# Kernel optimization log

Measured on AMD Instinct MI355X. Metric: run time of the kernel, lower is better.

Reference implementation:

```python
import jax, jax.numpy as jnp
import numpy as np

EMBED_DIM = 1024
NUM_HEADS = 16
HEAD_DIM = EMBED_DIM // NUM_HEADS
WINDOW_SIZE = 256
BATCH = 2
SEQ = 2048


def setup_inputs() -> dict:
    key = jax.random.key(0)
    ks = jax.random.split(key, 5)
    s = 1.0 / np.sqrt(EMBED_DIM)
    return {
        "x": jax.random.normal(ks[0], (BATCH, SEQ, EMBED_DIM), dtype=jnp.float32),
        "Wq": jax.random.normal(ks[1], (EMBED_DIM, EMBED_DIM), dtype=jnp.float32) * s,
        "Wk": jax.random.normal(ks[2], (EMBED_DIM, EMBED_DIM), dtype=jnp.float32) * s,
        "Wv": jax.random.normal(ks[3], (EMBED_DIM, EMBED_DIM), dtype=jnp.float32) * s,
        "Wo": jax.random.normal(ks[4], (EMBED_DIM, EMBED_DIM), dtype=jnp.float32) * s,
    }


def _split_heads(t):
    # [B, S, E] -> [B, H, S, D]
    b, s, _ = t.shape
    return t.reshape(b, s, NUM_HEADS, HEAD_DIM).transpose(0, 2, 1, 3)


def reference(x, Wq, Wk, Wv, Wo):
    b, s, _ = x.shape
    # nn.Linear(bias=False): y = x @ W.T
    q = _split_heads(x @ Wq.T)
    k = _split_heads(x @ Wk.T)
    v = _split_heads(x @ Wv.T)
    scores = jnp.einsum("bhqd,bhkd->bhqk", q, k) / np.sqrt(HEAD_DIM).astype(np.float32)
    i = jnp.arange(s)[:, None]
    j = jnp.arange(s)[None, :]
    # causal sliding window: attend to j in [i - window_size + 1, i]
    allowed = (j <= i) & (j >= i - WINDOW_SIZE + 1)
    scores = jnp.where(allowed[None, None], scores, -jnp.inf)
    probs = jax.nn.softmax(scores, axis=-1)
    ctx = jnp.einsum("bhqk,bhkd->bhqd", probs, v)  # [B,H,S,D]
    ctx = ctx.transpose(0, 2, 1, 3).reshape(b, s, EMBED_DIM)
    return ctx @ Wo.T
```

## Files before the change

kernel.cpp:

```cpp
#include <hip/hip_runtime.h>
#include <hip/hip_bf16.h>
#include <stdint.h>

#define EDIM 1024
#define NH 16
#define HD 64
#define WIN 256
#define BB 2
#define SS 2048
#define MR (BB*SS)
#define NQKV 3072

typedef __attribute__((ext_vector_type(8))) short short8;
typedef __attribute__((ext_vector_type(4))) float f32x4;

__device__ __forceinline__ unsigned short f2bf(float f) {
  union { float f; uint32_t u; } c; c.f = f;
  uint32_t r = (c.u + 0x7FFFu + ((c.u >> 16) & 1u)) >> 16;
  return (unsigned short)r;
}

__global__ __launch_bounds__(256) void cvt_kernel(const float* __restrict__ s,
                                                  unsigned short* __restrict__ d, int n8) {
  int i = blockIdx.x * 256 + threadIdx.x;
  if (i >= n8) return;
  const float4* s4 = (const float4*)s;
  float4 a = s4[2*i], b = s4[2*i+1];
  short8 o;
  o[0]=(short)f2bf(a.x); o[1]=(short)f2bf(a.y); o[2]=(short)f2bf(a.z); o[3]=(short)f2bf(a.w);
  o[4]=(short)f2bf(b.x); o[5]=(short)f2bf(b.y); o[6]=(short)f2bf(b.z); o[7]=(short)f2bf(b.w);
  ((short8*)d)[i] = o;
}

template<typename OutT>
__global__ __launch_bounds__(256) void gemm_bt(const unsigned short* __restrict__ A,
                                               const unsigned short* __restrict__ Bw,
                                               OutT* __restrict__ C, int M, int N, int K) {
  __shared__ unsigned short As[128*64];
  __shared__ unsigned short Bs[128*64];
  const int t = threadIdx.x, lane = t & 63;
  const int w = t >> 6, wr = w >> 1, wc = w & 1;
  const int m0 = blockIdx.y * 128, n0 = blockIdx.x * 128;
  f32x4 acc[4][4] = {};
  for (int kt = 0; kt < K; kt += 64) {
    __syncthreads();
#pragma unroll
    for (int r = 0; r < 4; ++r) {
      const int row = r*32 + (t >> 3);
      const int colb = (((t & 7) ^ (row & 7)) << 4);
      const int o = r*4096 + t*16;
      __builtin_amdgcn_global_load_lds(
        (const __attribute__((address_space(1))) char*)(A + (size_t)(m0 + row) * K + kt + (colb >> 1)),
        (__attribute__((address_space(3))) char*)((char*)As + o), 16, 0, 0);
      __builtin_amdgcn_global_load_lds(
        (const __attribute__((address_space(1))) char*)(Bw + (size_t)(n0 + row) * K + kt + (colb >> 1)),
        (__attribute__((address_space(3))) char*)((char*)Bs + o), 16, 0, 0);
    }
    __syncthreads();
#pragma unroll
    for (int c = 0; c < 2; ++c) {
      const int k0 = c*32 + ((lane >> 4) << 3);
      short8 af[4], bfr[4];
#pragma unroll
      for (int mi = 0; mi < 4; ++mi) {
        const int row = wr*64 + mi*16 + (lane & 15);
        const int off = ((row << 7) + (k0 << 1)) ^ ((row & 7) << 4);
        af[mi] = *(const short8*)((const char*)As + off);
      }
#pragma unroll
      for (int ni = 0; ni < 4; ++ni) {
        const int row = wc*64 + ni*16 + (lane & 15);
        const int off = ((row << 7) + (k0 << 1)) ^ ((row & 7) << 4);
        bfr[ni] = *(const short8*)((const char*)Bs + off);
      }
#pragma unroll
      for (int mi = 0; mi < 4; ++mi)
#pragma unroll
        for (int ni = 0; ni < 4; ++ni)
          acc[mi][ni] = __builtin_amdgcn_mfma_f32_16x16x32_bf16(af[mi], bfr[ni], acc[mi][ni], 0, 0, 0);
    }
  }
#pragma unroll
  for (int mi = 0; mi < 4; ++mi) {
    const int rb = m0 + wr*64 + mi*16 + ((lane >> 4) << 2);
#pragma unroll
    for (int ni = 0; ni < 4; ++ni) {
      const int col = n0 + wc*64 + ni*16 + (lane & 15);
#pragma unroll
      for (int reg = 0; reg < 4; ++reg) {
        const float v = acc[mi][ni][reg];
        const size_t idx = (size_t)(rb + reg) * N + col;
        if constexpr (sizeof(OutT) == 2) ((unsigned short*)C)[idx] = f2bf(v);
        else ((float*)C)[idx] = v;
      }
    }
  }
}

__global__ __launch_bounds__(256) void attn_kernel(const unsigned short* __restrict__ qkv,
                                                   unsigned short* __restrict__ ctx) {
  __shared__ unsigned short Ks[64*64];
  __shared__ unsigned short VTs[64*64];
  __shared__ unsigned short Ps[4][16*64];
  const int t = threadIdx.x, lane = t & 63, w = t >> 6;
  const int qt = blockIdx.x, bh = blockIdx.y;
  const int b = bh >> 4, h = bh & 15;
  const int q0 = qt << 6;
  const int qw0 = q0 + (w << 4);
  const unsigned short* qb = qkv + (size_t)b * SS * NQKV + h * HD;
  const unsigned short* kb = qb + EDIM;
  const unsigned short* vb = qb + 2*EDIM;
  short8 aq[2];
  {
    const size_t roff = (size_t)(qw0 + (lane & 15)) * NQKV + ((lane >> 4) << 3);
    aq[0] = *(const short8*)(qb + roff);
    aq[1] = *(const short8*)(qb + roff + 32);
  }
  f32x4 oacc[4] = {};
  float mrun[4], lrun[4];
#pragma unroll
  for (int r = 0; r < 4; ++r) { mrun[r] = -1e30f; lrun[r] = 0.f; }
  const int t_lo = qt >= 4 ? qt - 4 : 0;
  for (int kt = t_lo; kt <= qt; ++kt) {
    const int kv0 = kt << 6;
    __syncthreads();
#pragma unroll
    for (int r = 0; r < 2; ++r) {
      const int o = r*4096 + t*16;
      const int key = o >> 7;
      const int colb = (o & 127) ^ ((key & 7) << 4);
      __builtin_amdgcn_global_load_lds(
        (const __attribute__((address_space(1))) char*)(kb + (size_t)(kv0 + key) * NQKV + (colb >> 1)),
        (__attribute__((address_space(3))) char*)((char*)Ks + o), 16, 0, 0);
    }
#pragma unroll
    for (int i = 0; i < 2; ++i) {
      const int c = t + (i << 8);
      const int key = c >> 3;
      const int d0 = (c & 7) << 3;
      short8 vv = *(const short8*)(vb + (size_t)(kv0 + key) * NQKV + d0);
#pragma unroll
      for (int j = 0; j < 8; ++j) {
        const int d = d0 + j;
        const int off = ((d << 7) + (key << 1)) ^ ((d & 7) << 4);
        *(unsigned short*)((char*)VTs + off) = (unsigned short)(short)vv[j];
      }
    }
    __syncthreads();
    f32x4 sc[4] = {};
#pragma unroll
    for (int kf = 0; kf < 4; ++kf) {
#pragma unroll
      for (int c = 0; c < 2; ++c) {
        const int krow = (kf << 4) + (lane & 15);
        const int k0 = (c << 5) + ((lane >> 4) << 3);
        const int off = ((krow << 7) + (k0 << 1)) ^ ((krow & 7) << 4);
        short8 bk = *(const short8*)((const char*)Ks + off);
        sc[kf] = __builtin_amdgcn_mfma_f32_16x16x32_bf16(aq[c], bk, sc[kf], 0, 0, 0);
      }
    }
#pragma unroll
    for (int reg = 0; reg < 4; ++reg) {
      const int qg = qw0 + ((lane >> 4) << 2) + reg;
      float sv[4];
#pragma unroll
      for (int kf = 0; kf < 4; ++kf) {
        const int kg = kv0 + (kf << 4) + (lane & 15);
        const bool ok = (kg <= qg) && (kg + WIN > qg);
        sv[kf] = ok ? sc[kf][reg] * 0.125f : -1e30f;
      }
      float pm = fmaxf(fmaxf(sv[0], sv[1]), fmaxf(sv[2], sv[3]));
      pm = fmaxf(pm, __shfl_xor(pm, 1));
      pm = fmaxf(pm, __shfl_xor(pm, 2));
      pm = fmaxf(pm, __shfl_xor(pm, 4));
      pm = fmaxf(pm, __shfl_xor(pm, 8));
      const float mn = fmaxf(mrun[reg], pm);
      const float corr = __expf(mrun[reg] - mn);
      mrun[reg] = mn;
      float rs = 0.f;
      const int qrow = ((lane >> 4) << 2) + reg;
#pragma unroll
      for (int kf = 0; kf < 4; ++kf) {
        const float p = __expf(sv[kf] - mn);
        rs += p;
        const int key = (kf << 4) + (lane & 15);
        const int off = ((qrow << 7) + (key << 1)) ^ ((qrow & 7) << 4);
        *(unsigned short*)((char*)&Ps[w][0] + off) = f2bf(p);
      }
      rs += __shfl_xor(rs, 1);
      rs += __shfl_xor(rs, 2);
      rs += __shfl_xor(rs, 4);
      rs += __shfl_xor(rs, 8);
      lrun[reg] = lrun[reg] * corr + rs;
#pragma unroll
      for (int nf = 0; nf < 4; ++nf) oacc[nf][reg] *= corr;
    }
#pragma unroll
    for (int c2 = 0; c2 < 2; ++c2) {
      const int prow = lane & 15;
      const int k0 = (c2 << 5) + ((lane >> 4) << 3);
      const int offp = ((prow << 7) + (k0 << 1)) ^ ((prow & 7) << 4);
      short8 pa = *(const short8*)((const char*)&Ps[w][0] + offp);
#pragma unroll
      for (int nf = 0; nf < 4; ++nf) {
        const int d = (nf << 4) + (lane & 15);
        const int offv = ((d << 7) + (k0 << 1)) ^ ((d & 7) << 4);
        short8 bv = *(const short8*)((const char*)VTs + offv);
        oacc[nf] = __builtin_amdgcn_mfma_f32_16x16x32_bf16(pa, bv, oacc[nf], 0, 0, 0);
      }
    }
  }
  unsigned short* cb = ctx + (size_t)b * SS * EDIM + h * HD;
#pragma unroll
  for (int nf = 0; nf < 4; ++nf)
#pragma unroll
    for (int reg = 0; reg < 4; ++reg) {
      const int qg = qw0 + ((lane >> 4) << 2) + reg;
      const int d = (nf << 4) + (lane & 15);
      cb[(size_t)qg * EDIM + d] = f2bf(oacc[nf][reg] / lrun[reg]);
    }
}

extern "C" void kernel_launch(void* const* d_in, const int* in_sizes, int n_in,
                              void* d_out, int out_size, void* d_ws, size_t ws_size,
                              hipStream_t stream) {
  const float* x  = (const float*)d_in[0];
  const float* Wq = (const float*)d_in[1];
  const float* Wk = (const float*)d_in[2];
  const float* Wv = (const float*)d_in[3];
  const float* Wo = (const float*)d_in[4];
  float* out = (float*)d_out;
  char* ws = (char*)d_ws;
  unsigned short* xb   = (unsigned short*)(ws);
  unsigned short* ctxb = (unsigned short*)(ws);
  unsigned short* wqkv = (unsigned short*)(ws + (size_t)(8u << 20));
  unsigned short* wob  = (unsigned short*)(ws + (size_t)(14u << 20));
  unsigned short* qkv  = (unsigned short*)(ws + (size_t)(16u << 20));

  const int nx8 = (MR * EDIM) / 8;
  const int nw8 = (EDIM * EDIM) / 8;
  cvt_kernel<<<dim3(nx8 / 256), dim3(256), 0, stream>>>(x, xb, nx8);
  cvt_kernel<<<dim3(nw8 / 256), dim3(256), 0, stream>>>(Wq, wqkv, nw8);
  cvt_kernel<<<dim3(nw8 / 256), dim3(256), 0, stream>>>(Wk, wqkv + EDIM*EDIM, nw8);
  cvt_kernel<<<dim3(nw8 / 256), dim3(256), 0, stream>>>(Wv, wqkv + 2*EDIM*EDIM, nw8);
  cvt_kernel<<<dim3(nw8 / 256), dim3(256), 0, stream>>>(Wo, wob, nw8);

  gemm_bt<unsigned short><<<dim3(NQKV/128, MR/128), dim3(256), 0, stream>>>(
      xb, wqkv, qkv, MR, NQKV, EDIM);

  attn_kernel<<<dim3(SS/64, BB*NH), dim3(256), 0, stream>>>(qkv, ctxb);

  gemm_bt<float><<<dim3(EDIM/128, MR/128), dim3(256), 0, stream>>>(
      ctxb, wob, out, MR, EDIM, EDIM);
}
```

Baseline: 175.5 us.

## Fuse conversions, swizzle grids, use transposed LDS reads for V, retile output GEMM

Merges the five fp32-to-bf16 conversion launches into one kernel. The GEMMs and the attention kernel now use a 1D grid remapped so that consecutive blocks land on different XCDs. The output projection uses 128x64 tiles to raise the block count. In attention, V is loaded straight into LDS with global_load_lds in a permuted layout and read back with ds_read_b64_tr_b16, replacing the scalar transpose stores, and s_setprio is added around the MFMA sections. The gains come from fewer launches, better cache locality and cheaper V staging, at the cost of a fragile hand-computed layout that must exactly match the transposed-read semantics.

```diff
diff --git a/kernel.cpp b/kernel.cpp
--- a/kernel.cpp
+++ b/kernel.cpp
@@ -12,6 +12,7 @@
 #define NQKV 3072
 
 typedef __attribute__((ext_vector_type(8))) short short8;
+typedef __attribute__((ext_vector_type(4))) short short4v;
 typedef __attribute__((ext_vector_type(4))) float f32x4;
 
 __device__ __forceinline__ unsigned short f2bf(float f) {
@@ -20,38 +21,61 @@
   return (unsigned short)r;
 }
 
-__global__ __launch_bounds__(256) void cvt_kernel(const float* __restrict__ s,
-                                                  unsigned short* __restrict__ d, int n8) {
-  int i = blockIdx.x * 256 + threadIdx.x;
-  if (i >= n8) return;
+__global__ __launch_bounds__(256) void cvt_all(const float* __restrict__ x,
+                                               const float* __restrict__ Wq,
+                                               const float* __restrict__ Wk,
+                                               const float* __restrict__ Wv,
+                                               const float* __restrict__ Wo,
+                                               unsigned short* __restrict__ dst) {
+  const int i = blockIdx.x * 256 + threadIdx.x;
+  const float* s; int off;
+  if (i < 524288) { s = x; off = i; }
+  else {
+    const int j = i - 524288, wsel = j >> 17;
+    off = j & 131071;
+    s = wsel == 0 ? Wq : wsel == 1 ? Wk : wsel == 2 ? Wv : Wo;
+  }
   const float4* s4 = (const float4*)s;
-  float4 a = s4[2*i], b = s4[2*i+1];
+  float4 a = s4[2*off], b = s4[2*off+1];
   short8 o;
   o[0]=(short)f2bf(a.x); o[1]=(short)f2bf(a.y); o[2]=(short)f2bf(a.z); o[3]=(short)f2bf(a.w);
   o[4]=(short)f2bf(b.x); o[5]=(short)f2bf(b.y); o[6]=(short)f2bf(b.z); o[7]=(short)f2bf(b.w);
-  ((short8*)d)[i] = o;
-}
-
-template<typename OutT>
+  ((short8*)dst)[i] = o;
+}
+
+template<typename OutT, int BM, int BN>
 __global__ __launch_bounds__(256) void gemm_bt(const unsigned short* __restrict__ A,
                                                const unsigned short* __restrict__ Bw,
-                                               OutT* __restrict__ C, int M, int N, int K) {
-  __shared__ unsigned short As[128*64];
-  __shared__ unsigned short Bs[128*64];
+                                               OutT* __restrict__ C,
+                                               int M, int N, int K, int nbx) {
+  constexpr int MI = BM / 32;
+  constexpr int NI = BN / 32;
+  constexpr int LA = BM / 32;
+  constexpr int LB = BN / 32;
+  __shared__ unsigned short As[BM * 64];
+  __shared__ unsigned short Bs[BN * 64];
   const int t = threadIdx.x, lane = t & 63;
   const int w = t >> 6, wr = w >> 1, wc = w & 1;
-  const int m0 = blockIdx.y * 128, n0 = blockIdx.x * 128;
-  f32x4 acc[4][4] = {};
+  const int nwg = gridDim.x, bid = blockIdx.x;
+  const int wg = (bid & 7) * (nwg >> 3) + (bid >> 3);
+  const int m0 = (wg / nbx) * BM, n0 = (wg % nbx) * BN;
+  f32x4 acc[MI][NI] = {};
   for (int kt = 0; kt < K; kt += 64) {
     __syncthreads();
 #pragma unroll
-    for (int r = 0; r < 4; ++r) {
+    for (int r = 0; r < LA; ++r) {
       const int row = r*32 + (t >> 3);
       const int colb = (((t & 7) ^ (row & 7)) << 4);
       const int o = r*4096 + t*16;
       __builtin_amdgcn_global_load_lds(
         (const __attribute__((address_space(1))) char*)(A + (size_t)(m0 + row) * K + kt + (colb >> 1)),
         (__attribute__((address_space(3))) char*)((char*)As + o), 16, 0, 0);
+    }
+#pragma unroll
+    for (int r = 0; r < LB; ++r) {
+      const int row = r*32 + (t >> 3);
+      const int colb = (((t & 7) ^ (row & 7)) << 4);
+      const int o = r*4096 + t*16;
       __builtin_amdgcn_global_load_lds(
         (const __attribute__((address_space(1))) char*)(Bw + (size_t)(n0 + row) * K + kt + (colb >> 1)),
         (__attribute__((address_space(3))) char*)((char*)Bs + o), 16, 0, 0);
@@ -60,32 +84,32 @@
 #pragma unroll
     for (int c = 0; c < 2; ++c) {
       const int k0 = c*32 + ((lane >> 4) << 3);
-      short8 af[4], bfr[4];
-#pragma unroll
-      for (int mi = 0; mi < 4; ++mi) {
-        const int row = wr*64 + mi*16 + (lane & 15);
+      short8 af[MI], bfr[NI];
+#pragma unroll
+      for (int mi = 0; mi < MI; ++mi) {
+        const int row = wr*(BM/2) + mi*16 + (lane & 15);
         const int off = ((row << 7) + (k0 << 1)) ^ ((row & 7) << 4);
         af[mi] = *(const short8*)((const char*)As + off);
       }
 #pragma unroll
-      for (int ni = 0; ni < 4; ++ni) {
-        const int row = wc*64 + ni*16 + (lane & 15);
+      for (int ni = 0; ni < NI; ++ni) {
+        const int row = wc*(BN/2) + ni*16 + (lane & 15);
         const int off = ((row << 7) + (k0 << 1)) ^ ((row & 7) << 4);
         bfr[ni] = *(const short8*)((const char*)Bs + off);
       }
 #pragma unroll
-      for (int mi = 0; mi < 4; ++mi)
-#pragma unroll
-        for (int ni = 0; ni < 4; ++ni)
+      for (int mi = 0; mi < MI; ++mi)
+#pragma unroll
+        for (int ni = 0; ni < NI; ++ni)
           acc[mi][ni] = __builtin_amdgcn_mfma_f32_16x16x32_bf16(af[mi], bfr[ni], acc[mi][ni], 0, 0, 0);
     }
   }
 #pragma unroll
-  for (int mi = 0; mi < 4; ++mi) {
-    const int rb = m0 + wr*64 + mi*16 + ((lane >> 4) << 2);
-#pragma unroll
-    for (int ni = 0; ni < 4; ++ni) {
-      const int col = n0 + wc*64 + ni*16 + (lane & 15);
+  for (int mi = 0; mi < MI; ++mi) {
+    const int rb = m0 + wr*(BM/2) + mi*16 + ((lane >> 4) << 2);
+#pragma unroll
+    for (int ni = 0; ni < NI; ++ni) {
+      const int col = n0 + wc*(BN/2) + ni*16 + (lane & 15);
 #pragma unroll
       for (int reg = 0; reg < 4; ++reg) {
         const float v = acc[mi][ni][reg];
@@ -99,11 +123,13 @@
 
 __global__ __launch_bounds__(256) void attn_kernel(const unsigned short* __restrict__ qkv,
                                                    unsigned short* __restrict__ ctx) {
-  __shared__ unsigned short Ks[64*64];
-  __shared__ unsigned short VTs[64*64];
-  __shared__ unsigned short Ps[4][16*64];
+  __shared__ __align__(16) unsigned short Ks[64*64];
+  __shared__ __align__(16) unsigned short VTs[64*64];
+  __shared__ __align__(16) unsigned short Ps[4][16*64];
   const int t = threadIdx.x, lane = t & 63, w = t >> 6;
-  const int qt = blockIdx.x, bh = blockIdx.y;
+  const int bid = blockIdx.x;
+  const int swz = (bid & 7) * 128 + (bid >> 3);
+  const int qt = swz & 31, bh = swz >> 5;
   const int b = bh >> 4, h = bh & 15;
   const int q0 = qt << 6;
   const int qw0 = q0 + (w << 4);
@@ -116,6 +142,8 @@
     aq[0] = *(const short8*)(qb + roff);
     aq[1] = *(const short8*)(qb + roff + 32);
   }
+  const unsigned vt0 = (unsigned)(uintptr_t)(__attribute__((address_space(3))) char*)((char*)VTs);
+  const unsigned trbase = vt0 + ((lane & 15) << 3) + ((lane >> 4) << 7);
   f32x4 oacc[4] = {};
   float mrun[4], lrun[4];
 #pragma unroll
@@ -135,19 +163,17 @@
     }
 #pragma unroll
     for (int i = 0; i < 2; ++i) {
-      const int c = t + (i << 8);
-      const int key = c >> 3;
-      const int d0 = (c & 7) << 3;
-      short8 vv = *(const short8*)(vb + (size_t)(kv0 + key) * NQKV + d0);
-#pragma unroll
-      for (int j = 0; j < 8; ++j) {
-        const int d = d0 + j;
-        const int off = ((d << 7) + (key << 1)) ^ ((d & 7) << 4);
-        *(unsigned short*)((char*)VTs + off) = (unsigned short)(short)vv[j];
-      }
+      const int p8 = (w << 6) + lane + (i << 8);
+      const int band = p8 >> 7, rr = p8 & 127, ordv = rr >> 3, q8 = rr & 7;
+      const int k = ((ordv & 7) << 3) + ((ordv >> 3) << 2) + (q8 >> 1);
+      const int d = (band << 4) + ((q8 & 1) << 3);
+      __builtin_amdgcn_global_load_lds(
+        (const __attribute__((address_space(1))) char*)(vb + (size_t)(kv0 + k) * NQKV + d),
+        (__attribute__((address_space(3))) char*)((char*)VTs + p8*16), 16, 0, 0);
     }
     __syncthreads();
     f32x4 sc[4] = {};
+    __builtin_amdgcn_s_setprio(1);
 #pragma unroll
     for (int kf = 0; kf < 4; ++kf) {
 #pragma unroll
@@ -159,6 +185,7 @@
         sc[kf] = __builtin_amdgcn_mfma_f32_16x16x32_bf16(aq[c], bk, sc[kf], 0, 0, 0);
       }
     }
+    __builtin_amdgcn_s_setprio(0);
 #pragma unroll
     for (int reg = 0; reg < 4; ++reg) {
       const int qg = qw0 + ((lane >> 4) << 2) + reg;
@@ -201,13 +228,22 @@
       const int k0 = (c2 << 5) + ((lane >> 4) << 3);
       const int offp = ((prow << 7) + (k0 << 1)) ^ ((prow & 7) << 4);
       short8 pa = *(const short8*)((const char*)&Ps[w][0] + offp);
+      short4v lo[4], hi[4];
 #pragma unroll
       for (int nf = 0; nf < 4; ++nf) {
-        const int d = (nf << 4) + (lane & 15);
-        const int offv = ((d << 7) + (k0 << 1)) ^ ((d & 7) << 4);
-        short8 bv = *(const short8*)((const char*)VTs + offv);
+        const unsigned a1 = trbase + (nf << 11) + (c2 << 9);
+        asm volatile("ds_read_b64_tr_b16 %0, %1" : "=&v"(lo[nf]) : "v"(a1));
+        asm volatile("ds_read_b64_tr_b16 %0, %1 offset:1024" : "=&v"(hi[nf]) : "v"(a1));
+      }
+      asm volatile("s_waitcnt lgkmcnt(0)" ::: "memory");
+      __builtin_amdgcn_sched_barrier(0);
+      __builtin_amdgcn_s_setprio(1);
+#pragma unroll
+      for (int nf = 0; nf < 4; ++nf) {
+        short8 bv = __builtin_shufflevector(lo[nf], hi[nf], 0, 1, 2, 3, 4, 5, 6, 7);
         oacc[nf] = __builtin_amdgcn_mfma_f32_16x16x32_bf16(pa, bv, oacc[nf], 0, 0, 0);
       }
+      __builtin_amdgcn_s_setprio(0);
     }
   }
   unsigned short* cb = ctx + (size_t)b * SS * EDIM + h * HD;
@@ -237,19 +273,13 @@
   unsigned short* wob  = (unsigned short*)(ws + (size_t)(14u << 20));
   unsigned short* qkv  = (unsigned short*)(ws + (size_t)(16u << 20));
 
-  const int nx8 = (MR * EDIM) / 8;
-  const int nw8 = (EDIM * EDIM) / 8;
-  cvt_kernel<<<dim3(nx8 / 256), dim3(256), 0, stream>>>(x, xb, nx8);
-  cvt_kernel<<<dim3(nw8 / 256), dim3(256), 0, stream>>>(Wq, wqkv, nw8);
-  cvt_kernel<<<dim3(nw8 / 256), dim3(256), 0, stream>>>(Wk, wqkv + EDIM*EDIM, nw8);
-  cvt_kernel<<<dim3(nw8 / 256), dim3(256), 0, stream>>>(Wv, wqkv + 2*EDIM*EDIM, nw8);
-  cvt_kernel<<<dim3(nw8 / 256), dim3(256), 0, stream>>>(Wo, wob, nw8);
-
-  gemm_bt<unsigned short><<<dim3(NQKV/128, MR/128), dim3(256), 0, stream>>>(
-      xb, wqkv, qkv, MR, NQKV, EDIM);
-
-  attn_kernel<<<dim3(SS/64, BB*NH), dim3(256), 0, stream>>>(qkv, ctxb);
-
-  gemm_bt<float><<<dim3(EDIM/128, MR/128), dim3(256), 0, stream>>>(
-      ctxb, wob, out, MR, EDIM, EDIM);
-}
+  cvt_all<<<dim3(4096), dim3(256), 0, stream>>>(x, Wq, Wk, Wv, Wo, xb);
+
+  gemm_bt<unsigned short, 128, 128><<<dim3(768), dim3(256), 0, stream>>>(
+      xb, wqkv, qkv, MR, NQKV, EDIM, NQKV/128);
+
+  attn_kernel<<<dim3(1024), dim3(256), 0, stream>>>(qkv, ctxb);
+
+  gemm_bt<float, 128, 64><<<dim3(512), dim3(256), 0, stream>>>(
+      ctxb, wob, out, MR, EDIM, EDIM, EDIM/64);
+}
```

After: 161.4 us. -8.1%, faster.
